# Kernel tuning notes

Measured on AMD Instinct MI355X. Metric: run time of the kernel, lower is better.

The kernel has to match this reference:

```python
import jax, jax.numpy as jnp
import numpy as np

B, L, K, H = 4, 2048, 48, 128
FF = 4 * H
SCALE = 30.0
EPS = 1e-5


def layer_norm(x, g, b):
    m = jnp.mean(x, axis=-1, keepdims=True)
    v = jnp.mean(jnp.square(x - m), axis=-1, keepdims=True)
    return (x - m) * jax.lax.rsqrt(v + EPS) * g + b


def gelu(x):
    return jax.nn.gelu(x, approximate=False)  # torch.nn.GELU default (erf)


def gather_nodes(nodes, neighbor_idx):
    # nodes: [B,L,H], neighbor_idx: [B,L,K] -> [B,L,K,H]
    Bn, Ln, Kn = neighbor_idx.shape
    flat = neighbor_idx.reshape(Bn, Ln * Kn)
    out = jnp.take_along_axis(nodes, flat[:, :, None], axis=1)
    return out.reshape(Bn, Ln, Kn, nodes.shape[-1])


def setup_inputs() -> dict:
    key = jax.random.key(0)
    ks = jax.random.split(key, 32)
    s = 0.02
    def w(k, shape):
        return jax.random.normal(k, shape, jnp.float32) * s
    inp = {
        "h_V": jax.random.normal(ks[0], (B, L, H), jnp.float32),
        "h_E": jax.random.normal(ks[1], (B, L, K, H), jnp.float32),
        "E_idx": jax.random.randint(ks[2], (B, L, K), 0, L),
        "mask_V": jnp.ones((B, L), jnp.float32),
        "mask_attend": jnp.ones((B, L, K), jnp.float32),
        # message MLP (node update): W1,W2,W3 (stored as [in,out])
        "W1": w(ks[3], (3 * H, H)), "b1": jnp.zeros((H,), jnp.float32),
        "W2": w(ks[4], (H, H)),     "b2": jnp.zeros((H,), jnp.float32),
        "W3": w(ks[5], (H, H)),     "b3": jnp.zeros((H,), jnp.float32),
        # edge-update MLP: W11,W12,W13
        "W11": w(ks[6], (3 * H, H)), "b11": jnp.zeros((H,), jnp.float32),
        "W12": w(ks[7], (H, H)),     "b12": jnp.zeros((H,), jnp.float32),
        "W13": w(ks[8], (H, H)),     "b13": jnp.zeros((H,), jnp.float32),
        # position-wise FFN
        "Wg_in": w(ks[9], (H, FF)),  "bg_in": jnp.zeros((FF,), jnp.float32),
        "Wg_out": w(ks[10], (FF, H)), "bg_out": jnp.zeros((H,), jnp.float32),
        # LayerNorms
        "n1g": jnp.ones((H,), jnp.float32), "n1b": jnp.zeros((H,), jnp.float32),
        "n2g": jnp.ones((H,), jnp.float32), "n2b": jnp.zeros((H,), jnp.float32),
        "n3g": jnp.ones((H,), jnp.float32), "n3b": jnp.zeros((H,), jnp.float32),
    }
    return inp


def reference(h_V, h_E, E_idx, mask_V, mask_attend,
              W1, b1, W2, b2, W3, b3,
              W11, b11, W12, b12, W13, b13,
              Wg_in, bg_in, Wg_out, bg_out,
              n1g, n1b, n2g, n2b, n3g, n3b):
    # --- node update ---
    hv_nbr = gather_nodes(h_V, E_idx)                      # [B,L,K,H]
    h_V_exp = jnp.broadcast_to(h_V[:, :, None, :], hv_nbr.shape)
    h_EV = jnp.concatenate([h_V_exp, h_E, hv_nbr], -1)     # [B,L,K,3H]
    h_msg = gelu(h_EV @ W1 + b1)
    h_msg = gelu(h_msg @ W2 + b2)
    h_msg = h_msg @ W3 + b3
    h_msg = mask_attend[..., None] * h_msg
    dh = jnp.sum(h_msg, axis=-2) / SCALE                   # [B,L,H]
    h_V = layer_norm(h_V + dh, n1g, n1b)                   # dropout=eval (identity)
    dh = gelu(h_V @ Wg_in + bg_in) @ Wg_out + bg_out
    h_V = layer_norm(h_V + dh, n2g, n2b)
    h_V = mask_V[..., None] * h_V
    # --- edge update ---
    hv_nbr2 = gather_nodes(h_V, E_idx)
    h_V_exp2 = jnp.broadcast_to(h_V[:, :, None, :], hv_nbr2.shape)
    h_EV2 = jnp.concatenate([h_V_exp2, h_E, hv_nbr2], -1)  # [B,L,K,3H]
    h_msg2 = gelu(h_EV2 @ W11 + b11)
    h_msg2 = gelu(h_msg2 @ W12 + b12)
    h_msg2 = h_msg2 @ W13 + b13
    h_E = layer_norm(h_E + h_msg2, n3g, n3b)
    return (h_V, h_E)
```

## Files before the change

kernel.cpp:

```cpp
#include <hip/hip_runtime.h>


typedef __attribute__((ext_vector_type(8))) short short8;
typedef __attribute__((ext_vector_type(4))) float f32x4;

#define MFMA16(a,b,c) __builtin_amdgcn_mfma_f32_16x16x32_bf16((a),(b),(c),0,0,0)

#define L_SEQ 2048
#define K_NBR 48
#define H_DIM 128

__device__ __forceinline__ unsigned cvtpk(float lo, float hi){
  unsigned r;
  asm("v_cvt_pk_bf16_f32 %0, %1, %2" : "=v"(r) : "v"(lo), "v"(hi));
  return r;
}
__device__ __forceinline__ unsigned short f2bf(float x){ return (unsigned short)cvtpk(x, x); }
__device__ __forceinline__ float bflo(unsigned u){ return __uint_as_float(u << 16); }
__device__ __forceinline__ float bfhi(unsigned u){ return __uint_as_float(u & 0xffff0000u); }

__device__ __forceinline__ float gelu_f(float x){
  float t = fmaf(x * x, 0.044715f, 1.0f);
  float e = __builtin_amdgcn_exp2f(-2.3022082f * x * t);
  return x * __builtin_amdgcn_rcpf(1.0f + e);
}

__global__ void k_wt(const float* __restrict__ in, unsigned short* __restrict__ out,
                     int R, int C){
  int o = blockIdx.x * 256 + threadIdx.x;
  int c = o / R, r = o - c * R;
  out[o] = f2bf(in[r * C + c]);
}

__global__ void k_cvt16(const float* __restrict__ in, unsigned short* __restrict__ out){
  int i = blockIdx.x * 256 + threadIdx.x;
  float4 v = ((const float4*)in)[i];
  uint2 p;
  p.x = cvtpk(v.x, v.y);
  p.y = cvtpk(v.z, v.w);
  ((uint2*)out)[i] = p;
}

__global__ __launch_bounds__(256, 6) void k_node(
  const float* __restrict__ hV, const float* __restrict__ hE,
  const unsigned short* __restrict__ hV16,
  const int* __restrict__ Eidx, const float* __restrict__ maskA,
  const unsigned short* __restrict__ Wt1, const float* __restrict__ b1,
  const unsigned short* __restrict__ Wt2, const float* __restrict__ b2,
  const unsigned short* __restrict__ Wt3, const float* __restrict__ b3,
  const float* __restrict__ n1g, const float* __restrict__ n1b,
  float* __restrict__ v32, unsigned short* __restrict__ v16)
{
  __shared__ __align__(16) short Abuf[13056];
  __shared__ __align__(16) float aux[256];

  const int tid  = threadIdx.x;
  const int node = blockIdx.x;
  const int b    = node >> 11;

  if (tid < 128) aux[tid] = hV[(size_t)node * H_DIM + tid];

  const float4* srcE = (const float4*)(hE + (size_t)node * K_NBR * H_DIM);
  #pragma unroll
  for (int ii = 0; ii < 6; ++ii) {
    int i = tid + ii * 256;
    float4 v = srcE[i];
    int r = i >> 5, c = (i & 31) << 2;
    uint2 p; p.x = cvtpk(v.x, v.y); p.y = cvtpk(v.z, v.w);
    *(uint2*)&Abuf[r * 264 + c] = p;
  }
  const int* eip = Eidx + (size_t)node * K_NBR;
  #pragma unroll
  for (int ii = 0; ii < 6; ++ii) {
    int i = tid + ii * 256;
    int r = i >> 5, c = i & 31;
    int e = eip[r];
    *(uint2*)&Abuf[r * 264 + 128 + (c << 2)] =
        ((const uint2*)(hV16 + ((size_t)(b * L_SEQ) + e) * H_DIM))[c];
  }
  __syncthreads();

  if (tid < 128) {
    float acc = b1[tid];
    const unsigned* w = (const unsigned*)(Wt1 + (size_t)tid * 384);
    const float4* h4 = (const float4*)aux;
    #pragma unroll 8
    for (int j = 0; j < 32; ++j) {
      float4 hh = h4[j];
      unsigned w0 = w[2 * j], w1 = w[2 * j + 1];
      acc = fmaf(hh.x, bflo(w0), acc);
      acc = fmaf(hh.y, bfhi(w0), acc);
      acc = fmaf(hh.z, bflo(w1), acc);
      acc = fmaf(hh.w, bfhi(w1), acc);
    }
    aux[128 + tid] = acc;
  }

  const int wid = tid >> 6, lane = tid & 63;
  const int lr = lane & 15, lg = lane >> 4, kele = lg * 8;

  f32x4 zero = {0.f, 0.f, 0.f, 0.f};
  f32x4 acc[3][2];
  #pragma unroll
  for (int t = 0; t < 3; ++t)
    #pragma unroll
    for (int n = 0; n < 2; ++n) acc[t][n] = zero;

  #pragma unroll 2
  for (int kk = 0; kk < 8; ++kk) {
    short8 a0 = *(const short8*)&Abuf[(lr     ) * 264 + kk * 32 + kele];
    short8 a1 = *(const short8*)&Abuf[(lr + 16) * 264 + kk * 32 + kele];
    short8 a2 = *(const short8*)&Abuf[(lr + 32) * 264 + kk * 32 + kele];
    #pragma unroll
    for (int n = 0; n < 2; ++n) {
      short8 bf = *(const short8*)(const void*)(Wt1 + (size_t)(wid * 32 + n * 16 + lr) * 384 + 128 + kk * 32 + kele);
      acc[0][n] = MFMA16(a0, bf, acc[0][n]);
      acc[1][n] = MFMA16(a1, bf, acc[1][n]);
      acc[2][n] = MFMA16(a2, bf, acc[2][n]);
    }
  }
  __syncthreads();
  #pragma unroll
  for (int t = 0; t < 3; ++t)
    #pragma unroll
    for (int n = 0; n < 2; ++n) {
      int col = wid * 32 + n * 16 + lr;
      float sb = aux[128 + col];
      #pragma unroll
      for (int r = 0; r < 4; ++r) {
        int row = t * 16 + lg * 4 + r;
        Abuf[row * 136 + col] = (short)cvtpk(gelu_f(acc[t][n][r] + sb), 0.f);
      }
    }
  __syncthreads();

  #pragma unroll
  for (int t = 0; t < 3; ++t)
    #pragma unroll
    for (int n = 0; n < 2; ++n) acc[t][n] = zero;
  #pragma unroll
  for (int kk = 0; kk < 4; ++kk) {
    short8 a0 = *(const short8*)&Abuf[(lr     ) * 136 + kk * 32 + kele];
    short8 a1 = *(const short8*)&Abuf[(lr + 16) * 136 + kk * 32 + kele];
    short8 a2 = *(const short8*)&Abuf[(lr + 32) * 136 + kk * 32 + kele];
    #pragma unroll
    for (int n = 0; n < 2; ++n) {
      short8 bf = *(const short8*)(const void*)(Wt2 + (size_t)(wid * 32 + n * 16 + lr) * 128 + kk * 32 + kele);
      acc[0][n] = MFMA16(a0, bf, acc[0][n]);
      acc[1][n] = MFMA16(a1, bf, acc[1][n]);
      acc[2][n] = MFMA16(a2, bf, acc[2][n]);
    }
  }
  #pragma unroll
  for (int t = 0; t < 3; ++t)
    #pragma unroll
    for (int n = 0; n < 2; ++n) {
      int col = wid * 32 + n * 16 + lr;
      float bb = b2[col];
      #pragma unroll
      for (int r = 0; r < 4; ++r) {
        int row = t * 16 + lg * 4 + r;
        Abuf[6528 + row * 136 + col] = (short)cvtpk(gelu_f(acc[t][n][r] + bb), 0.f);
      }
    }
  __syncthreads();

  #pragma unroll
  for (int t = 0; t < 3; ++t)
    #pragma unroll
    for (int n = 0; n < 2; ++n) acc[t][n] = zero;
  #pragma unroll
  for (int kk = 0; kk < 4; ++kk) {
    short8 a0 = *(const short8*)&Abuf[6528 + (lr     ) * 136 + kk * 32 + kele];
    short8 a1 = *(const short8*)&Abuf[6528 + (lr + 16) * 136 + kk * 32 + kele];
    short8 a2 = *(const short8*)&Abuf[6528 + (lr + 32) * 136 + kk * 32 + kele];
    #pragma unroll
    for (int n = 0; n < 2; ++n) {
      short8 bf = *(const short8*)(const void*)(Wt3 + (size_t)(wid * 32 + n * 16 + lr) * 128 + kk * 32 + kele);
      acc[0][n] = MFMA16(a0, bf, acc[0][n]);
      acc[1][n] = MFMA16(a1, bf, acc[1][n]);
      acc[2][n] = MFMA16(a2, bf, acc[2][n]);
    }
  }
  const float* mrow = maskA + (size_t)node * K_NBR;
  float mk[3][4];
  #pragma unroll
  for (int t = 0; t < 3; ++t)
    #pragma unroll
    for (int r = 0; r < 4; ++r) mk[t][r] = mrow[t * 16 + lg * 4 + r];
  float part[2];
  #pragma unroll
  for (int n = 0; n < 2; ++n) {
    int col = wid * 32 + n * 16 + lr;
    float bb = b3[col];
    float p = 0.f;
    #pragma unroll
    for (int t = 0; t < 3; ++t)
      #pragma unroll
      for (int r = 0; r < 4; ++r)
        p += (acc[t][n][r] + bb) * mk[t][r];
    part[n] = p;
  }
  #pragma unroll
  for (int n = 0; n < 2; ++n) {
    part[n] += __shfl_xor(part[n], 16);
    part[n] += __shfl_xor(part[n], 32);
  }
  if (lane < 16) {
    #pragma unroll
    for (int n = 0; n < 2; ++n)
      aux[128 + wid * 32 + n * 16 + lane] = part[n] * (1.f / 30.f);
  }
  __syncthreads();

  if (wid == 0) {
    float u0 = aux[lane]      + aux[128 + lane];
    float u1 = aux[lane + 64] + aux[192 + lane];
    float s1 = u0 + u1, s2 = u0 * u0 + u1 * u1;
    #pragma unroll
    for (int off = 1; off < 64; off <<= 1) {
      s1 += __shfl_xor(s1, off);
      s2 += __shfl_xor(s2, off);
    }
    float mean = s1 * 0.0078125f;
    float var  = fmaf(s2, 0.0078125f, -mean * mean);
    float rs = rsqrtf(var + 1e-5f);
    float vv0 = (u0 - mean) * rs * n1g[lane]      + n1b[lane];
    float vv1 = (u1 - mean) * rs * n1g[lane + 64] + n1b[lane + 64];
    v32[(size_t)node * 128 + lane]      = vv0;
    v32[(size_t)node * 128 + lane + 64] = vv1;
    v16[(size_t)node * 128 + lane]      = f2bf(vv0);
    v16[(size_t)node * 128 + lane + 64] = f2bf(vv1);
  }
}

__global__ __launch_bounds__(256, 4) void k_ffn(
  const unsigned short* __restrict__ v16,
  const unsigned short* __restrict__ Wtgi, const float* __restrict__ bgi,
  const unsigned short* __restrict__ Wtgo, const float* __restrict__ bgo,
  const float* __restrict__ v32,
  const float* __restrict__ n2g, const float* __restrict__ n2b,
  const float* __restrict__ maskV, float* __restrict__ outV)
{
  __shared__ __align__(16) short Av[2176];
  __shared__ __align__(16) short Xb[8320];
  float* U = (float*)Xb;
  const int tid = threadIdx.x;
  const int row0 = blockIdx.x * 16;
  const uint2* src = (const uint2*)(v16 + (size_t)row0 * H_DIM);
  for (int i = tid; i < 512; i += 256) {
    int r = i >> 5, c = (i & 31) << 2;
    *(uint2*)&Av[r * 136 + c] = src[i];
  }
  __syncthreads();
  const int wid = tid >> 6, lane = tid & 63;
  const int lr = lane & 15, lg = lane >> 4, kele = lg * 8;
  f32x4 zero = {0.f, 0.f, 0.f, 0.f};
  f32x4 acc[8];
  #pragma unroll
  for (int n = 0; n < 8; ++n) acc[n] = zero;
  #pragma unroll
  for (int kk = 0; kk < 4; ++kk) {
    short8 a = *(const short8*)&Av[lr * 136 + kk * 32 + kele];
    #pragma unroll
    for (int n = 0; n < 8; ++n) {
      short8 bf = *(const short8*)(const void*)(Wtgi + (size_t)(wid * 128 + n * 16 + lr) * 128 + kk * 32 + kele);
      acc[n] = MFMA16(a, bf, acc[n]);
    }
  }
  #pragma unroll
  for (int n = 0; n < 8; ++n) {
    int col = wid * 128 + n * 16 + lr;
    float bb = bgi[col];
    #pragma unroll
    for (int r = 0; r < 4; ++r) {
      int row = lg * 4 + r;
      Xb[row * 520 + col] = (short)cvtpk(gelu_f(acc[n][r] + bb), 0.f);
    }
  }
  __syncthreads();
  f32x4 acc2[2];
  #pragma unroll
  for (int n = 0; n < 2; ++n) acc2[n] = zero;
  #pragma unroll 4
  for (int kk = 0; kk < 16; ++kk) {
    short8 a = *(const short8*)&Xb[lr * 520 + kk * 32 + kele];
    #pragma unroll
    for (int n = 0; n < 2; ++n) {
      short8 bf = *(const short8*)(const void*)(Wtgo + (size_t)(wid * 32 + n * 16 + lr) * 512 + kk * 32 + kele);
      acc2[n] = MFMA16(a, bf, acc2[n]);
    }
  }
  __syncthreads();
  #pragma unroll
  for (int n = 0; n < 2; ++n) {
    int col = wid * 32 + n * 16 + lr;
    float bb = bgo[col];
    #pragma unroll
    for (int r = 0; r < 4; ++r) {
      int row = lg * 4 + r;
      U[row * 132 + col] = acc2[n][r] + bb + v32[(size_t)(row0 + row) * 128 + col];
    }
  }
  __syncthreads();
  if (tid < 128) {
    int r = tid >> 3, sub = tid & 7;
    const float* Ur = &U[r * 132 + sub * 16];
    float u[16]; float s1 = 0.f, s2 = 0.f;
    #pragma unroll
    for (int i = 0; i < 16; ++i) { u[i] = Ur[i]; s1 += u[i]; s2 += u[i] * u[i]; }
    s1 += __shfl_xor(s1, 1); s1 += __shfl_xor(s1, 2); s1 += __shfl_xor(s1, 4);
    s2 += __shfl_xor(s2, 1); s2 += __shfl_xor(s2, 2); s2 += __shfl_xor(s2, 4);
    float mean = s1 * 0.0078125f;
    float var  = fmaf(s2, 0.0078125f, -mean * mean);
    float rs = rsqrtf(var + 1e-5f);
    int nd = row0 + r;
    float mv = maskV[nd];
    float* dst = outV + (size_t)nd * 128 + sub * 16;
    #pragma unroll
    for (int i = 0; i < 16; ++i) {
      int c = sub * 16 + i;
      dst[i] = ((u[i] - mean) * rs * n2g[c] + n2b[c]) * mv;
    }
  }
}

__global__ __launch_bounds__(256, 6) void k_edge(
  const float* __restrict__ hE, const int* __restrict__ Eidx,
  const float* __restrict__ hVn,
  const unsigned short* __restrict__ Wt11, const float* __restrict__ b11,
  const unsigned short* __restrict__ Wt12, const float* __restrict__ b12,
  const unsigned short* __restrict__ Wt13, const float* __restrict__ b13,
  const float* __restrict__ n3g, const float* __restrict__ n3b,
  float* __restrict__ outE)
{
  __shared__ __align__(16) short Abuf[13056];
  __shared__ __align__(16) float aux[256];
  float* MSG = (float*)Abuf;

  const int tid  = threadIdx.x;
  const int node = blockIdx.x;
  const int b    = node >> 11;

  if (tid < 128) aux[tid] = hVn[(size_t)node * H_DIM + tid];

  const float4* srcE = (const float4*)(hE + (size_t)node * K_NBR * H_DIM);
  #pragma unroll
  for (int ii = 0; ii < 6; ++ii) {
    int i = tid + ii * 256;
    float4 v = srcE[i];
    int r = i >> 5, c = (i & 31) << 2;
    uint2 p; p.x = cvtpk(v.x, v.y); p.y = cvtpk(v.z, v.w);
    *(uint2*)&Abuf[r * 264 + c] = p;
  }
  const int* eip = Eidx + (size_t)node * K_NBR;
  #pragma unroll
  for (int ii = 0; ii < 6; ++ii) {
    int i = tid + ii * 256;
    int r = i >> 5, c = i & 31;
    int e = eip[r];
    float4 v = ((const float4*)(hVn + ((size_t)(b * L_SEQ) + e) * H_DIM))[c];
    uint2 p; p.x = cvtpk(v.x, v.y); p.y = cvtpk(v.z, v.w);
    *(uint2*)&Abuf[r * 264 + 128 + (c << 2)] = p;
  }
  __syncthreads();

  if (tid < 128) {
    float acc = b11[tid];
    const unsigned* w = (const unsigned*)(Wt11 + (size_t)tid * 384);
    const float4* h4 = (const float4*)aux;
    #pragma unroll 8
    for (int j = 0; j < 32; ++j) {
      float4 hh = h4[j];
      unsigned w0 = w[2 * j], w1 = w[2 * j + 1];
      acc = fmaf(hh.x, bflo(w0), acc);
      acc = fmaf(hh.y, bfhi(w0), acc);
      acc = fmaf(hh.z, bflo(w1), acc);
      acc = fmaf(hh.w, bfhi(w1), acc);
    }
    aux[128 + tid] = acc;
  }

  const int wid = tid >> 6, lane = tid & 63;
  const int lr = lane & 15, lg = lane >> 4, kele = lg * 8;

  f32x4 zero = {0.f, 0.f, 0.f, 0.f};
  f32x4 acc[3][2];
  #pragma unroll
  for (int t = 0; t < 3; ++t)
    #pragma unroll
    for (int n = 0; n < 2; ++n) acc[t][n] = zero;

  #pragma unroll 2
  for (int kk = 0; kk < 8; ++kk) {
    short8 a0 = *(const short8*)&Abuf[(lr     ) * 264 + kk * 32 + kele];
    short8 a1 = *(const short8*)&Abuf[(lr + 16) * 264 + kk * 32 + kele];
    short8 a2 = *(const short8*)&Abuf[(lr + 32) * 264 + kk * 32 + kele];
    #pragma unroll
    for (int n = 0; n < 2; ++n) {
      short8 bf = *(const short8*)(const void*)(Wt11 + (size_t)(wid * 32 + n * 16 + lr) * 384 + 128 + kk * 32 + kele);
      acc[0][n] = MFMA16(a0, bf, acc[0][n]);
      acc[1][n] = MFMA16(a1, bf, acc[1][n]);
      acc[2][n] = MFMA16(a2, bf, acc[2][n]);
    }
  }
  __syncthreads();
  #pragma unroll
  for (int t = 0; t < 3; ++t)
    #pragma unroll
    for (int n = 0; n < 2; ++n) {
      int col = wid * 32 + n * 16 + lr;
      float sb = aux[128 + col];
      #pragma unroll
      for (int r = 0; r < 4; ++r) {
        int row = t * 16 + lg * 4 + r;
        Abuf[row * 136 + col] = (short)cvtpk(gelu_f(acc[t][n][r] + sb), 0.f);
      }
    }
  __syncthreads();
  if (tid < 128) {
    aux[tid]       = n3g[tid];
    aux[128 + tid] = n3b[tid];
  }

  #pragma unroll
  for (int t = 0; t < 3; ++t)
    #pragma unroll
    for (int n = 0; n < 2; ++n) acc[t][n] = zero;
  #pragma unroll
  for (int kk = 0; kk < 4; ++kk) {
    short8 a0 = *(const short8*)&Abuf[(lr     ) * 136 + kk * 32 + kele];
    short8 a1 = *(const short8*)&Abuf[(lr + 16) * 136 + kk * 32 + kele];
    short8 a2 = *(const short8*)&Abuf[(lr + 32) * 136 + kk * 32 + kele];
    #pragma unroll
    for (int n = 0; n < 2; ++n) {
      short8 bf = *(const short8*)(const void*)(Wt12 + (size_t)(wid * 32 + n * 16 + lr) * 128 + kk * 32 + kele);
      acc[0][n] = MFMA16(a0, bf, acc[0][n]);
      acc[1][n] = MFMA16(a1, bf, acc[1][n]);
      acc[2][n] = MFMA16(a2, bf, acc[2][n]);
    }
  }
  #pragma unroll
  for (int t = 0; t < 3; ++t)
    #pragma unroll
    for (int n = 0; n < 2; ++n) {
      int col = wid * 32 + n * 16 + lr;
      float bb = b12[col];
      #pragma unroll
      for (int r = 0; r < 4; ++r) {
        int row = t * 16 + lg * 4 + r;
        Abuf[6528 + row * 136 + col] = (short)cvtpk(gelu_f(acc[t][n][r] + bb), 0.f);
      }
    }
  __syncthreads();

  #pragma unroll
  for (int t = 0; t < 3; ++t)
    #pragma unroll
    for (int n = 0; n < 2; ++n) acc[t][n] = zero;
  #pragma unroll
  for (int kk = 0; kk < 4; ++kk) {
    short8 a0 = *(const short8*)&Abuf[6528 + (lr     ) * 136 + kk * 32 + kele];
    short8 a1 = *(const short8*)&Abuf[6528 + (lr + 16) * 136 + kk * 32 + kele];
    short8 a2 = *(const short8*)&Abuf[6528 + (lr + 32) * 136 + kk * 32 + kele];
    #pragma unroll
    for (int n = 0; n < 2; ++n) {
      short8 bf = *(const short8*)(const void*)(Wt13 + (size_t)(wid * 32 + n * 16 + lr) * 128 + kk * 32 + kele);
      acc[0][n] = MFMA16(a0, bf, acc[0][n]);
      acc[1][n] = MFMA16(a1, bf, acc[1][n]);
      acc[2][n] = MFMA16(a2, bf, acc[2][n]);
    }
  }
  __syncthreads();
  #pragma unroll
  for (int t = 0; t < 3; ++t)
    #pragma unroll
    for (int n = 0; n < 2; ++n) {
      int col = wid * 32 + n * 16 + lr;
      float bb = b13[col];
      #pragma unroll
      for (int r = 0; r < 4; ++r) {
        int row = t * 16 + lg * 4 + r;
        MSG[row * 132 + col] = acc[t][n][r] + bb;
      }
    }
  __syncthreads();

  if (tid < 96) {
    int rr = tid >> 1, half = tid & 1;
    size_t ebase = ((size_t)node * K_NBR + rr) * H_DIM;
    const float4* he4 = (const float4*)(hE + ebase) + half * 16;
    const float4* m4  = (const float4*)(MSG + rr * 132) + half * 16;
    float s1 = 0.f, s2 = 0.f;
    #pragma unroll 4
    for (int i = 0; i < 16; ++i) {
      float4 a = he4[i]; float4 mm = m4[i];
      float x0 = a.x + mm.x, x1 = a.y + mm.y, x2 = a.z + mm.z, x3 = a.w + mm.w;
      s1 += x0 + x1 + x2 + x3;
      s2 += x0 * x0 + x1 * x1 + x2 * x2 + x3 * x3;
    }
    s1 += __shfl_xor(s1, 1);
    s2 += __shfl_xor(s2, 1);
    float mean = s1 * 0.0078125f;
    float var  = fmaf(s2, 0.0078125f, -mean * mean);
    float rs = rsqrtf(var + 1e-5f);
    float4* dst = (float4*)(outE + ebase) + half * 16;
    #pragma unroll 4
    for (int i = 0; i < 16; ++i) {
      float4 a = he4[i]; float4 mm = m4[i];
      int c = half * 64 + i * 4;
      float4 o;
      o.x = (a.x + mm.x - mean) * rs * aux[c + 0] + aux[128 + c + 0];
      o.y = (a.y + mm.y - mean) * rs * aux[c + 1] + aux[128 + c + 1];
      o.z = (a.z + mm.z - mean) * rs * aux[c + 2] + aux[128 + c + 2];
      o.w = (a.w + mm.w - mean) * rs * aux[c + 3] + aux[128 + c + 3];
      dst[i] = o;
    }
  }
}

extern "C" void kernel_launch(void* const* d_in, const int* in_sizes, int n_in,
                              void* d_out, int out_size, void* d_ws, size_t ws_size,
                              hipStream_t stream) {
  const float* hV   = (const float*)d_in[0];
  const float* hE   = (const float*)d_in[1];
  const int*   Eidx = (const int*)d_in[2];
  const float* maskV= (const float*)d_in[3];
  const float* maskA= (const float*)d_in[4];
  const float* W1 = (const float*)d_in[5];  const float* b1 = (const float*)d_in[6];
  const float* W2 = (const float*)d_in[7];  const float* b2 = (const float*)d_in[8];
  const float* W3 = (const float*)d_in[9];  const float* b3 = (const float*)d_in[10];
  const float* W11= (const float*)d_in[11]; const float* b11= (const float*)d_in[12];
  const float* W12= (const float*)d_in[13]; const float* b12= (const float*)d_in[14];
  const float* W13= (const float*)d_in[15]; const float* b13= (const float*)d_in[16];
  const float* Wgi= (const float*)d_in[17]; const float* bgi= (const float*)d_in[18];
  const float* Wgo= (const float*)d_in[19]; const float* bgo= (const float*)d_in[20];
  const float* n1g= (const float*)d_in[21]; const float* n1b= (const float*)d_in[22];
  const float* n2g= (const float*)d_in[23]; const float* n2b= (const float*)d_in[24];
  const float* n3g= (const float*)d_in[25]; const float* n3b= (const float*)d_in[26];

  float* outV = (float*)d_out;
  float* outE = outV + (size_t)4 * 2048 * 128;

  unsigned short* wsu  = (unsigned short*)d_ws;
  unsigned short* Wt1  = wsu + 0;
  unsigned short* Wt2  = wsu + 49152;
  unsigned short* Wt3  = wsu + 65536;
  unsigned short* Wt11 = wsu + 81920;
  unsigned short* Wt12 = wsu + 131072;
  unsigned short* Wt13 = wsu + 147456;
  unsigned short* Wtgi = wsu + 163840;
  unsigned short* Wtgo = wsu + 229376;

  char* scr = (char*)outE;
  unsigned short* hV16 = (unsigned short*)scr;
  float*          v32  = (float*)(scr + (size_t)2097152);
  unsigned short* v16  = (unsigned short*)(scr + (size_t)6291456);

  k_wt<<<192, 256, 0, stream>>>(W1,  Wt1,  384, 128);
  k_wt<<<64,  256, 0, stream>>>(W2,  Wt2,  128, 128);
  k_wt<<<64,  256, 0, stream>>>(W3,  Wt3,  128, 128);
  k_wt<<<192, 256, 0, stream>>>(W11, Wt11, 384, 128);
  k_wt<<<64,  256, 0, stream>>>(W12, Wt12, 128, 128);
  k_wt<<<64,  256, 0, stream>>>(W13, Wt13, 128, 128);
  k_wt<<<256, 256, 0, stream>>>(Wgi, Wtgi, 128, 512);
  k_wt<<<256, 256, 0, stream>>>(Wgo, Wtgo, 512, 128);
  k_cvt16<<<1024, 256, 0, stream>>>(hV, hV16);

  k_node<<<8192, 256, 0, stream>>>(hV, hE, hV16, Eidx, maskA,
                                   Wt1, b1, Wt2, b2, Wt3, b3, n1g, n1b, v32, v16);
  k_ffn<<<512, 256, 0, stream>>>(v16, Wtgi, bgi, Wtgo, bgo, v32,
                                 n2g, n2b, maskV, outV);
  k_edge<<<8192, 256, 0, stream>>>(hE, Eidx, outV,
                                   Wt11, b11, Wt12, b12, Wt13, b13, n3g, n3b, outE);
}
```

Before: 826.6 us.

## Compute self-node projection with MFMA, widen edge layernorm, relax launch bounds

The per-node h_V·W1[0:128] projection was a scalar FMA loop run by half the threads, with its result added as a bias. It is now folded into the MFMA accumulation by broadcasting the bf16 self-node vector as the A operand for all row tiles. The edge layer-norm epilogue is spread over 192 threads (4 per row) instead of 96, and both kernels relax launch_bounds min-blocks from 6 to 4. This removes a serial scalar phase but spends redundant MFMAs on an identical A operand and converts the self term to bf16. The new launch bound permits more registers per thread, possibly at the cost of occupancy.

```diff
diff --git a/kernel.cpp b/kernel.cpp
--- a/kernel.cpp
+++ b/kernel.cpp
@@ -16,8 +16,6 @@
   return r;
 }
 __device__ __forceinline__ unsigned short f2bf(float x){ return (unsigned short)cvtpk(x, x); }
-__device__ __forceinline__ float bflo(unsigned u){ return __uint_as_float(u << 16); }
-__device__ __forceinline__ float bfhi(unsigned u){ return __uint_as_float(u & 0xffff0000u); }
 
 __device__ __forceinline__ float gelu_f(float x){
   float t = fmaf(x * x, 0.044715f, 1.0f);
@@ -41,7 +39,7 @@
   ((uint2*)out)[i] = p;
 }
 
-__global__ __launch_bounds__(256, 6) void k_node(
+__global__ __launch_bounds__(256, 4) void k_node(
   const float* __restrict__ hV, const float* __restrict__ hE,
   const unsigned short* __restrict__ hV16,
   const int* __restrict__ Eidx, const float* __restrict__ maskA,
@@ -52,6 +50,7 @@
   float* __restrict__ v32, unsigned short* __restrict__ v16)
 {
   __shared__ __align__(16) short Abuf[13056];
+  __shared__ __align__(16) short hvs[128];
   __shared__ __align__(16) float aux[256];
 
   const int tid  = threadIdx.x;
@@ -59,6 +58,8 @@
   const int b    = node >> 11;
 
   if (tid < 128) aux[tid] = hV[(size_t)node * H_DIM + tid];
+  if (tid < 32)
+    ((uint2*)hvs)[tid] = ((const uint2*)(hV16 + (size_t)node * H_DIM))[tid];
 
   const float4* srcE = (const float4*)(hE + (size_t)node * K_NBR * H_DIM);
   #pragma unroll
@@ -80,22 +81,6 @@
   }
   __syncthreads();
 
-  if (tid < 128) {
-    float acc = b1[tid];
-    const unsigned* w = (const unsigned*)(Wt1 + (size_t)tid * 384);
-    const float4* h4 = (const float4*)aux;
-    #pragma unroll 8
-    for (int j = 0; j < 32; ++j) {
-      float4 hh = h4[j];
-      unsigned w0 = w[2 * j], w1 = w[2 * j + 1];
-      acc = fmaf(hh.x, bflo(w0), acc);
-      acc = fmaf(hh.y, bfhi(w0), acc);
-      acc = fmaf(hh.z, bflo(w1), acc);
-      acc = fmaf(hh.w, bfhi(w1), acc);
-    }
-    aux[128 + tid] = acc;
-  }
-
   const int wid = tid >> 6, lane = tid & 63;
   const int lr = lane & 15, lg = lane >> 4, kele = lg * 8;
 
@@ -106,6 +91,17 @@
     #pragma unroll
     for (int n = 0; n < 2; ++n) acc[t][n] = zero;
 
+  #pragma unroll
+  for (int kk = 0; kk < 4; ++kk) {
+    short8 as = *(const short8*)&hvs[kk * 32 + kele];
+    #pragma unroll
+    for (int n = 0; n < 2; ++n) {
+      short8 bf = *(const short8*)(const void*)(Wt1 + (size_t)(wid * 32 + n * 16 + lr) * 384 + kk * 32 + kele);
+      acc[0][n] = MFMA16(as, bf, acc[0][n]);
+      acc[1][n] = MFMA16(as, bf, acc[1][n]);
+      acc[2][n] = MFMA16(as, bf, acc[2][n]);
+    }
+  }
   #pragma unroll 2
   for (int kk = 0; kk < 8; ++kk) {
     short8 a0 = *(const short8*)&Abuf[(lr     ) * 264 + kk * 32 + kele];
@@ -125,11 +121,11 @@
     #pragma unroll
     for (int n = 0; n < 2; ++n) {
       int col = wid * 32 + n * 16 + lr;
-      float sb = aux[128 + col];
+      float bb = b1[col];
       #pragma unroll
       for (int r = 0; r < 4; ++r) {
         int row = t * 16 + lg * 4 + r;
-        Abuf[row * 136 + col] = (short)cvtpk(gelu_f(acc[t][n][r] + sb), 0.f);
+        Abuf[row * 136 + col] = (short)cvtpk(gelu_f(acc[t][n][r] + bb), 0.f);
       }
     }
   __syncthreads();
@@ -325,7 +321,7 @@
   }
 }
 
-__global__ __launch_bounds__(256, 6) void k_edge(
+__global__ __launch_bounds__(256, 4) void k_edge(
   const float* __restrict__ hE, const int* __restrict__ Eidx,
   const float* __restrict__ hVn,
   const unsigned short* __restrict__ Wt11, const float* __restrict__ b11,
@@ -335,6 +331,7 @@
   float* __restrict__ outE)
 {
   __shared__ __align__(16) short Abuf[13056];
+  __shared__ __align__(16) short hvs[128];
   __shared__ __align__(16) float aux[256];
   float* MSG = (float*)Abuf;
 
@@ -342,7 +339,15 @@
   const int node = blockIdx.x;
   const int b    = node >> 11;
 
-  if (tid < 128) aux[tid] = hVn[(size_t)node * H_DIM + tid];
+  if (tid < 128) {
+    aux[tid]       = n3g[tid];
+    aux[128 + tid] = n3b[tid];
+  }
+  if (tid < 32) {
+    float4 v = ((const float4*)(hVn + (size_t)node * H_DIM))[tid];
+    uint2 p; p.x = cvtpk(v.x, v.y); p.y = cvtpk(v.z, v.w);
+    ((uint2*)hvs)[tid] = p;
+  }
 
   const float4* srcE = (const float4*)(hE + (size_t)node * K_NBR * H_DIM);
   #pragma unroll
@@ -365,22 +370,6 @@
   }
   __syncthreads();
 
-  if (tid < 128) {
-    float acc = b11[tid];
-    const unsigned* w = (const unsigned*)(Wt11 + (size_t)tid * 384);
-    const float4* h4 = (const float4*)aux;
-    #pragma unroll 8
-    for (int j = 0; j < 32; ++j) {
-      float4 hh = h4[j];
-      unsigned w0 = w[2 * j], w1 = w[2 * j + 1];
-      acc = fmaf(hh.x, bflo(w0), acc);
-      acc = fmaf(hh.y, bfhi(w0), acc);
-      acc = fmaf(hh.z, bflo(w1), acc);
-      acc = fmaf(hh.w, bfhi(w1), acc);
-    }
-    aux[128 + tid] = acc;
-  }
-
   const int wid = tid >> 6, lane = tid & 63;
   const int lr = lane & 15, lg = lane >> 4, kele = lg * 8;
 
@@ -391,6 +380,17 @@
     #pragma unroll
     for (int n = 0; n < 2; ++n) acc[t][n] = zero;
 
+  #pragma unroll
+  for (int kk = 0; kk < 4; ++kk) {
+    short8 as = *(const short8*)&hvs[kk * 32 + kele];
+    #pragma unroll
+    for (int n = 0; n < 2; ++n) {
+      short8 bf = *(const short8*)(const void*)(Wt11 + (size_t)(wid * 32 + n * 16 + lr) * 384 + kk * 32 + kele);
+      acc[0][n] = MFMA16(as, bf, acc[0][n]);
+      acc[1][n] = MFMA16(as, bf, acc[1][n]);
+      acc[2][n] = MFMA16(as, bf, acc[2][n]);
+    }
+  }
   #pragma unroll 2
   for (int kk = 0; kk < 8; ++kk) {
     short8 a0 = *(const short8*)&Abuf[(lr     ) * 264 + kk * 32 + kele];
@@ -410,18 +410,14 @@
     #pragma unroll
     for (int n = 0; n < 2; ++n) {
       int col = wid * 32 + n * 16 + lr;
-      float sb = aux[128 + col];
+      float bb = b11[col];
       #pragma unroll
       for (int r = 0; r < 4; ++r) {
         int row = t * 16 + lg * 4 + r;
-        Abuf[row * 136 + col] = (short)cvtpk(gelu_f(acc[t][n][r] + sb), 0.f);
+        Abuf[row * 136 + col] = (short)cvtpk(gelu_f(acc[t][n][r] + bb), 0.f);
       }
     }
   __syncthreads();
-  if (tid < 128) {
-    aux[tid]       = n3g[tid];
-    aux[128 + tid] = n3b[tid];
-  }
 
   #pragma unroll
   for (int t = 0; t < 3; ++t)
@@ -486,29 +482,29 @@
     }
   __syncthreads();
 
-  if (tid < 96) {
-    int rr = tid >> 1, half = tid & 1;
+  if (tid < 192) {
+    int rr = tid >> 2, q = tid & 3;
     size_t ebase = ((size_t)node * K_NBR + rr) * H_DIM;
-    const float4* he4 = (const float4*)(hE + ebase) + half * 16;
-    const float4* m4  = (const float4*)(MSG + rr * 132) + half * 16;
+    const float4* he4 = (const float4*)(hE + ebase) + q * 8;
+    const float4* m4  = (const float4*)(MSG + rr * 132) + q * 8;
     float s1 = 0.f, s2 = 0.f;
-    #pragma unroll 4
-    for (int i = 0; i < 16; ++i) {
+    #pragma unroll
+    for (int i = 0; i < 8; ++i) {
       float4 a = he4[i]; float4 mm = m4[i];
       float x0 = a.x + mm.x, x1 = a.y + mm.y, x2 = a.z + mm.z, x3 = a.w + mm.w;
       s1 += x0 + x1 + x2 + x3;
       s2 += x0 * x0 + x1 * x1 + x2 * x2 + x3 * x3;
     }
-    s1 += __shfl_xor(s1, 1);
-    s2 += __shfl_xor(s2, 1);
+    s1 += __shfl_xor(s1, 1); s1 += __shfl_xor(s1, 2);
+    s2 += __shfl_xor(s2, 1); s2 += __shfl_xor(s2, 2);
     float mean = s1 * 0.0078125f;
     float var  = fmaf(s2, 0.0078125f, -mean * mean);
     float rs = rsqrtf(var + 1e-5f);
-    float4* dst = (float4*)(outE + ebase) + half * 16;
-    #pragma unroll 4
-    for (int i = 0; i < 16; ++i) {
+    float4* dst = (float4*)(outE + ebase) + q * 8;
+    #pragma unroll
+    for (int i = 0; i < 8; ++i) {
       float4 a = he4[i]; float4 mm = m4[i];
-      int c = half * 64 + i * 4;
+      int c = q * 32 + i * 4;
       float4 o;
       o.x = (a.x + mm.x - mean) * rs * aux[c + 0] + aux[128 + c + 0];
       o.y = (a.y + mm.y - mean) * rs * aux[c + 1] + aux[128 + c + 1];
```

Result: faster. 783.2 us (-5.3%).
